# Optimization experiments

Measured on AMD Instinct MI355X. Metric: run time of the kernel, lower is better.

The kernel has to match this reference:

```python
import jax, jax.numpy as jnp
from jax import lax
import numpy as np

EPS = 1e-5
RADIUS = 0.2
NPOINT = 1024
NSAMPLE = 32
B, N = 8, 8192


def furthest_point_sample(xyz, npoint):
    # xyz: (B,N,3) -> idx (B,npoint), start at index 0 (pytorch3d default)
    Bn, Nn, _ = xyz.shape
    def step(carry, _):
        dists, last = carry  # (B,N), (B,)
        lastpt = jnp.take_along_axis(xyz, last[:, None, None], axis=1)  # (B,1,3)
        d = jnp.sum((xyz - lastpt) ** 2, axis=-1)  # (B,N)
        dists = jnp.minimum(dists, d)
        nxt = jnp.argmax(dists, axis=-1).astype(jnp.int32)
        return (dists, nxt), last
    init = (jnp.full((Bn, Nn), jnp.inf, xyz.dtype), jnp.zeros((Bn,), jnp.int32))
    _, idxs = lax.scan(step, init, None, length=npoint)  # (npoint,B)
    return idxs.T  # (B,npoint)


def ball_query(radius, nsample, xyz, new_xyz):
    # first `nsample` points (by original index order) within radius; pad -> 0 (clamp of -1)
    Nn = xyz.shape[1]
    d2 = jnp.sum((new_xyz[:, :, None, :] - xyz[:, None, :, :]) ** 2, axis=-1)  # (B,S,N)
    valid = d2 < radius * radius
    score = jnp.where(valid, jnp.arange(Nn, dtype=jnp.int32), jnp.int32(Nn))  # smaller = earlier valid
    neg_vals, _ = lax.top_k(-score, nsample)  # picks nsample smallest scores
    idx = -neg_vals  # (B,S,nsample)
    idx = jnp.where(idx == Nn, 0, idx)  # pytorch3d pads with -1, then clamp(min=0) -> 0
    return idx


def bn_relu(x, g, be, m, v):
    # eval-mode BatchNorm over channel (last) dim + ReLU
    return jax.nn.relu((x - m) * (g / jnp.sqrt(v + EPS)) + be)


def setup_inputs() -> dict:
    key = jax.random.key(0)
    ks = jax.random.split(key, 4)
    xyz = jax.random.uniform(ks[0], (B, N, 3), dtype=jnp.float32)
    w1 = jax.random.normal(ks[1], (64, 3), dtype=jnp.float32) * 0.1
    w2 = jax.random.normal(ks[2], (64, 64), dtype=jnp.float32) * 0.1
    w3 = jax.random.normal(ks[3], (128, 64), dtype=jnp.float32) * 0.1
    z64, o64 = jnp.zeros((64,), jnp.float32), jnp.ones((64,), jnp.float32)
    z128, o128 = jnp.zeros((128,), jnp.float32), jnp.ones((128,), jnp.float32)
    return {
        "xyz": xyz,
        "w1": w1, "b1": z64, "g1": o64, "be1": z64, "m1": z64, "v1": o64,
        "w2": w2, "b2": z64, "g2": o64, "be2": z64, "m2": z64, "v2": o64,
        "w3": w3, "b3": z128, "g3": o128, "be3": z128, "m3": z128, "v3": o128,
    }


def reference(xyz, w1, b1, g1, be1, m1, v1, w2, b2, g2, be2, m2, v2, w3, b3, g3, be3, m3, v3):
    fps_idx = furthest_point_sample(xyz, NPOINT)  # (B,npoint)
    new_xyz = jnp.take_along_axis(xyz, fps_idx[:, :, None], axis=1)  # (B,npoint,3)
    idx = ball_query(RADIUS, NSAMPLE, xyz, new_xyz)  # (B,npoint,nsample)
    grouped_xyz = jax.vmap(lambda pts, i: pts[i])(xyz, idx)  # (B,npoint,nsample,3)
    # 1x1 conv MLP (channels-last) + eval BN + ReLU
    h = bn_relu(jnp.einsum('bsnc,oc->bsno', grouped_xyz, w1) + b1, g1, be1, m1, v1)
    h = bn_relu(jnp.einsum('bsnc,oc->bsno', h, w2) + b2, g2, be2, m2, v2)
    h = bn_relu(jnp.einsum('bsnc,oc->bsno', h, w3) + b3, g3, be3, m3, v3)
    new_features = jnp.max(h, axis=2)  # (B,npoint,128) max over nsample
    new_features = jnp.transpose(new_features, (0, 2, 1))  # (B,128,npoint) to match torch layout
    return new_xyz, new_features
```

## Files before the change

### kernel.cpp

```cpp
#include <hip/hip_runtime.h>

#define B 8
#define N 8192
#define S 1024
#define NS 32
#define THREADS 256
#define NCONS_BLK 248
#define NCONS_WAVE (NCONS_BLK * 4)
constexpr float BN_EPS = 1e-5f;

typedef float v2f __attribute__((ext_vector_type(2)));

struct KParams {
  const float* xyz;
  const float *w1, *b1, *g1, *be1, *m1, *v1;
  const float *w2, *b2, *g2, *be2, *m2, *v2;
  const float *w3, *b3, *g3, *be3, *m3, *v3;
  float* new_xyz;
  float* out_feat;
  float* ctrs;
  unsigned* prog;
};

__device__ __forceinline__ float wave_max_to_lane63(float x) {
  int v = __float_as_int(x);
#define DPP_MAX(ctrl)                                                     \
  v = __float_as_int(fmaxf(__int_as_float(v),                             \
      __int_as_float(__builtin_amdgcn_update_dpp(v, v, (ctrl), 0xf, 0xf, \
                                                 false))))
  DPP_MAX(0x111);
  DPP_MAX(0x112);
  DPP_MAX(0x114);
  DPP_MAX(0x118);
  DPP_MAX(0x142);
  DPP_MAX(0x143);
#undef DPP_MAX
  return __int_as_float(v);
}

__device__ __forceinline__ void producer(const KParams& P, char* smem, int b,
                                         int t, int lane, int w) {
#pragma clang fp contract(off)
  float4* s_xyz4 = (float4*)smem;
  float* s_ctr = (float*)(smem + 131072);
  unsigned long long(*s_red)[4] =
      (unsigned long long(*)[4])(smem + 131072 + 12288);
  const float* base = P.xyz + (size_t)b * N * 3;
  v2f X[16], Y[16], Z[16], D[16];
  const int p0 = t * 32;
  {
    const float4* src = (const float4*)(base + (size_t)p0 * 3);
    float buf[96];
#pragma unroll
    for (int i = 0; i < 24; ++i) {
      float4 v = src[i];
      buf[4 * i + 0] = v.x; buf[4 * i + 1] = v.y;
      buf[4 * i + 2] = v.z; buf[4 * i + 3] = v.w;
    }
#pragma unroll
    for (int k = 0; k < 32; ++k)
      s_xyz4[p0 + k] =
          make_float4(buf[3 * k], buf[3 * k + 1], buf[3 * k + 2], 0.f);
#pragma unroll
    for (int i = 0; i < 16; ++i) {
      X[i] = (v2f){buf[6 * i + 0], buf[6 * i + 3]};
      Y[i] = (v2f){buf[6 * i + 1], buf[6 * i + 4]};
      Z[i] = (v2f){buf[6 * i + 2], buf[6 * i + 5]};
      D[i] = (v2f){3.4e38f, 3.4e38f};
    }
  }
  float lx = base[0], ly = base[1], lz = base[2];
  if (t == 0) { s_ctr[0] = lx; s_ctr[1] = ly; s_ctr[2] = lz; }
  for (int r = 1; r < S; ++r) {
    v2f lx2 = lx, ly2 = ly, lz2 = lz;
#pragma unroll
    for (int i = 0; i < 16; ++i) {
      v2f dx = X[i] - lx2, dy = Y[i] - ly2, dz = Z[i] - lz2;
      v2f d = (dx * dx + dy * dy) + dz * dz;
      D[i] = __builtin_elementwise_min(D[i], d);
    }
    float n1[16], n2[8], n3[4], n4[2];
#pragma unroll
    for (int i = 0; i < 16; ++i) n1[i] = fmaxf(D[i].x, D[i].y);
#pragma unroll
    for (int i = 0; i < 8; ++i) n2[i] = fmaxf(n1[2 * i], n1[2 * i + 1]);
#pragma unroll
    for (int i = 0; i < 4; ++i) n3[i] = fmaxf(n2[2 * i], n2[2 * i + 1]);
    n4[0] = fmaxf(n3[0], n3[1]);
    n4[1] = fmaxf(n3[2], n3[3]);
    float m = fmaxf(n4[0], n4[1]);
    int c4 = (n4[0] < m) ? 1 : 0;
    float n3s = c4 ? n3[2] : n3[0];
    int c3 = (n3s < m) ? 1 : 0;
    float n2a = c4 ? n2[4] : n2[0];
    float n2b = c4 ? n2[6] : n2[2];
    float n2s = c3 ? n2b : n2a;
    int c2 = (n2s < m) ? 1 : 0;
    float n1a = c4 ? n1[8] : n1[0];
    float n1b = c4 ? n1[10] : n1[2];
    float n1c = c4 ? n1[12] : n1[4];
    float n1d = c4 ? n1[14] : n1[6];
    float n1e = c3 ? n1c : n1a;
    float n1f = c3 ? n1d : n1b;
    float n1s = c2 ? n1f : n1e;
    int c1 = (n1s < m) ? 1 : 0;
    float e0 = c4 ? D[8].x : D[0].x;
    float e1 = c4 ? D[9].x : D[1].x;
    float e2 = c4 ? D[10].x : D[2].x;
    float e3 = c4 ? D[11].x : D[3].x;
    float e4 = c4 ? D[12].x : D[4].x;
    float e5 = c4 ? D[13].x : D[5].x;
    float e6 = c4 ? D[14].x : D[6].x;
    float e7 = c4 ? D[15].x : D[7].x;
    float f0 = c3 ? e4 : e0;
    float f1 = c3 ? e5 : e1;
    float f2 = c3 ? e6 : e2;
    float f3 = c3 ? e7 : e3;
    float g0 = c2 ? f2 : f0;
    float g1 = c2 ? f3 : f1;
    float dxs = c1 ? g1 : g0;
    int c0 = (dxs < m) ? 1 : 0;
    int li = 16 * c4 + 8 * c3 + 4 * c2 + 2 * c1 + c0;
    float wm = wave_max_to_lane63(m);
    float wavemax =
        __int_as_float(__builtin_amdgcn_readlane(__float_as_int(wm), 63));
    unsigned long long bal = __ballot(m == wavemax);
    int firstlane = (int)__builtin_ctzll(bal);
    int widx = __builtin_amdgcn_readlane(p0 + li, firstlane);
    unsigned long long key =
        ((unsigned long long)__float_as_uint(wavemax) << 32) |
        (unsigned)(8191 - widx);
    if (lane == 0) s_red[r & 1][w] = key;
    __syncthreads();
    {
      const unsigned long long* sr = s_red[r & 1];
      unsigned long long k0 = sr[0], k1 = sr[1], k2 = sr[2], k3 = sr[3];
      unsigned long long a = k0 > k1 ? k0 : k1;
      unsigned long long c = k2 > k3 ? k2 : k3;
      unsigned long long kmax = a > c ? a : c;
      const int bi = 8191 - (int)(unsigned)(kmax & 0xffffffffull);
      float4 cc = s_xyz4[bi];
      lx = cc.x; ly = cc.y; lz = cc.z;
    }
    if (t == 0) {
      s_ctr[r * 3 + 0] = lx; s_ctr[r * 3 + 1] = ly; s_ctr[r * 3 + 2] = lz;
    }
    if (w == 0 && (r & 7) == 7) {
      int k8 = r >> 3;
      if (lane == 0 && k8 >= 1)
        __hip_atomic_store(&P.prog[b * 64], (unsigned)(k8 * 8),
                           __ATOMIC_RELEASE, __HIP_MEMORY_SCOPE_AGENT);
      int cbase = (r - 7) * 3;
      if (lane < 24)
        __hip_atomic_store(P.ctrs + (size_t)b * (S * 3) + cbase + lane,
                           s_ctr[cbase + lane], __ATOMIC_RELAXED,
                           __HIP_MEMORY_SCOPE_AGENT);
    }
  }
  __syncthreads();
  if (w == 0 && lane == 0)
    __hip_atomic_store(&P.prog[b * 64], (unsigned)S, __ATOMIC_RELEASE,
                       __HIP_MEMORY_SCOPE_AGENT);
  float* o = P.new_xyz + (size_t)b * S * 3;
  for (int i = t; i < (S * 3) / 4; i += THREADS)
    ((float4*)o)[i] = ((const float4*)s_ctr)[i];
}

__device__ __forceinline__ void consumer(const KParams& P, char* smem, int cid,
                                         int t, int lane, int w) {
#pragma clang fp contract(off)
  constexpr float R2 = (float)(0.2 * 0.2);
  float* h = (float*)smem + w * (NS * 64);
  float* cs = (float*)smem + 4 * NS * 64 + w * (NS * 4);
  const unsigned gw = cid * 4 + w;
  float sv1 = P.g1[lane] / sqrtf(P.v1[lane] + BN_EPS);
  float bb1 = (P.b1[lane] - P.m1[lane]) * sv1 + P.be1[lane];
  float w1x = P.w1[lane * 3 + 0] * sv1, w1y = P.w1[lane * 3 + 1] * sv1,
        w1z = P.w1[lane * 3 + 2] * sv1;
  float sv2 = P.g2[lane] / sqrtf(P.v2[lane] + BN_EPS);
  float bb2 = (P.b2[lane] - P.m2[lane]) * sv2 + P.be2[lane];
  float W2[64];
#pragma unroll
  for (int k = 0; k < 64; k += 4) {
    float4 q = *(const float4*)(P.w2 + lane * 64 + k);
    W2[k + 0] = q.x * sv2; W2[k + 1] = q.y * sv2;
    W2[k + 2] = q.z * sv2; W2[k + 3] = q.w * sv2;
  }
  float sva = P.g3[lane] / sqrtf(P.v3[lane] + BN_EPS);
  float bba = (P.b3[lane] - P.m3[lane]) * sva + P.be3[lane];
  float svb = P.g3[lane + 64] / sqrtf(P.v3[lane + 64] + BN_EPS);
  float bbb = (P.b3[lane + 64] - P.m3[lane + 64]) * svb + P.be3[lane + 64];
  float Wa[64], Wb[64];
#pragma unroll
  for (int k = 0; k < 64; k += 4) {
    float4 qa = *(const float4*)(P.w3 + lane * 64 + k);
    Wa[k + 0] = qa.x * sva; Wa[k + 1] = qa.y * sva;
    Wa[k + 2] = qa.z * sva; Wa[k + 3] = qa.w * sva;
    float4 qb = *(const float4*)(P.w3 + (lane + 64) * 64 + k);
    Wb[k + 0] = qb.x * svb; Wb[k + 1] = qb.y * svb;
    Wb[k + 2] = qb.z * svb; Wb[k + 3] = qb.w * svb;
  }
  for (unsigned c = gw; c < B * S; c += NCONS_WAVE) {
    const int b = c & 7;
    const int s = c >> 3;
    while (__hip_atomic_load(&P.prog[b * 64], __ATOMIC_RELAXED,
                             __HIP_MEMORY_SCOPE_AGENT) <= (unsigned)s)
      __builtin_amdgcn_s_sleep(8);
    (void)__hip_atomic_load(&P.prog[b * 64], __ATOMIC_ACQUIRE,
                            __HIP_MEMORY_SCOPE_AGENT);
    const float* cg = P.ctrs + (size_t)b * (S * 3) + s * 3;
    float cx = __hip_atomic_load(cg + 0, __ATOMIC_RELAXED,
                                 __HIP_MEMORY_SCOPE_AGENT);
    float cy = __hip_atomic_load(cg + 1, __ATOMIC_RELAXED,
                                 __HIP_MEMORY_SCOPE_AGENT);
    float cz = __hip_atomic_load(cg + 2, __ATOMIC_RELAXED,
                                 __HIP_MEMORY_SCOPE_AGENT);
    const float* base = P.xyz + (size_t)b * N * 3;
    int cnt = 0;
    for (int c0 = 0; c0 < N && cnt < NS; c0 += 64) {
      int p = c0 + lane;
      float x = base[p * 3], y = base[p * 3 + 1], z = base[p * 3 + 2];
      float dx = x - cx, dy = y - cy, dz = z - cz;
      float d = (dx * dx + dy * dy) + dz * dz;
      bool v = d < R2;
      unsigned long long mk = __ballot(v);
      int rank = cnt + __popcll(mk & ((1ull << lane) - 1ull));
      if (v && rank < NS) {
        cs[rank * 4 + 0] = x; cs[rank * 4 + 1] = y; cs[rank * 4 + 2] = z;
      }
      cnt += (int)__popcll(mk);
    }
    if (cnt < NS) {
      float x0 = base[0], y0 = base[1], z0 = base[2];
      for (int j = cnt + lane; j < NS; j += 64) {
        cs[j * 4 + 0] = x0; cs[j * 4 + 1] = y0; cs[j * 4 + 2] = z0;
      }
    }
    for (int n = 0; n < NS; ++n) {
      float a = fmaf(w1x, cs[n * 4 + 0],
                     fmaf(w1y, cs[n * 4 + 1], fmaf(w1z, cs[n * 4 + 2], bb1)));
      h[n * 64 + lane] = fmaxf(a, 0.f);
    }
    for (int n = 0; n < NS; ++n) {
      float acc = bb2;
#pragma unroll
      for (int k = 0; k < 64; k += 4) {
        float4 q = *(const float4*)(h + n * 64 + k);
        acc = fmaf(W2[k + 0], q.x, acc);
        acc = fmaf(W2[k + 1], q.y, acc);
        acc = fmaf(W2[k + 2], q.z, acc);
        acc = fmaf(W2[k + 3], q.w, acc);
      }
      h[n * 64 + lane] = fmaxf(acc, 0.f);
    }
    float mxa = 0.f, mxb = 0.f;
    for (int n = 0; n < NS; ++n) {
      float acca = bba, accb = bbb;
#pragma unroll
      for (int k = 0; k < 64; k += 4) {
        float4 q = *(const float4*)(h + n * 64 + k);
        acca = fmaf(Wa[k + 0], q.x, acca);
        acca = fmaf(Wa[k + 1], q.y, acca);
        acca = fmaf(Wa[k + 2], q.z, acca);
        acca = fmaf(Wa[k + 3], q.w, acca);
        accb = fmaf(Wb[k + 0], q.x, accb);
        accb = fmaf(Wb[k + 1], q.y, accb);
        accb = fmaf(Wb[k + 2], q.z, accb);
        accb = fmaf(Wb[k + 3], q.w, accb);
      }
      mxa = fmaxf(mxa, acca);
      mxb = fmaxf(mxb, accb);
    }
    P.out_feat[((size_t)b * 128 + lane) * S + s] = mxa;
    P.out_feat[((size_t)b * 128 + 64 + lane) * S + s] = mxb;
  }
}

__global__ void __attribute__((amdgpu_flat_work_group_size(THREADS, THREADS),
                               amdgpu_waves_per_eu(1, 1)))
k_fused(KParams P) {
  extern __shared__ char smem[];
  const int t = threadIdx.x;
  const int lane = t & 63;
  const int w = t >> 6;
  if (blockIdx.x < B)
    producer(P, smem, blockIdx.x, t, lane, w);
  else
    consumer(P, smem, blockIdx.x - B, t, lane, w);
}

extern "C" void kernel_launch(void* const* d_in, const int* in_sizes, int n_in,
                              void* d_out, int out_size, void* d_ws,
                              size_t ws_size, hipStream_t stream) {
  KParams P;
  P.xyz = (const float*)d_in[0];
  P.w1 = (const float*)d_in[1];  P.b1 = (const float*)d_in[2];
  P.g1 = (const float*)d_in[3];  P.be1 = (const float*)d_in[4];
  P.m1 = (const float*)d_in[5];  P.v1 = (const float*)d_in[6];
  P.w2 = (const float*)d_in[7];  P.b2 = (const float*)d_in[8];
  P.g2 = (const float*)d_in[9];  P.be2 = (const float*)d_in[10];
  P.m2 = (const float*)d_in[11]; P.v2 = (const float*)d_in[12];
  P.w3 = (const float*)d_in[13]; P.b3 = (const float*)d_in[14];
  P.g3 = (const float*)d_in[15]; P.be3 = (const float*)d_in[16];
  P.m3 = (const float*)d_in[17]; P.v3 = (const float*)d_in[18];
  float* out = (float*)d_out;
  P.new_xyz = out;
  P.out_feat = out + (size_t)B * S * 3;
  P.prog = (unsigned*)d_ws;
  P.ctrs = (float*)((char*)d_ws + 2048);

  hipMemsetAsync(d_ws, 0, 2048, stream);

  void* args[] = {&P};
  dim3 grid(B + NCONS_BLK), blk(THREADS);
  size_t shmem = 131072 + 12288 + 256;
  hipError_t e = hipLaunchCooperativeKernel((const void*)k_fused, grid, blk,
                                            args, (unsigned)shmem, stream);
  if (e != hipSuccess) {
    k_fused<<<grid, blk, shmem, stream>>>(P);
  }
}
```

Measured before the change: 950.4 us.

## Replace per-iteration block barrier in FPS with tagged LDS spin-wait reduction

Each FPS iteration's workgroup __syncthreads is replaced by a flag-free exchange: every wave writes a key tagged with the iteration number to LDS, then spins with acquire loads until the other three waves' keys carry the same tag, and each wave computes the argmax itself. The point index is packed into 13 bits alongside the tag, and the key still orders by distance first. This removes a full barrier from the 1023-step serial critical path at the cost of spin traffic on LDS. The cooperative launch is also dropped for a plain launch, which no longer guarantees co-residency for the producer/consumer progress waits.

```diff
diff --git a/kernel.cpp b/kernel.cpp
--- a/kernel.cpp
+++ b/kernel.cpp
@@ -43,8 +43,8 @@
 #pragma clang fp contract(off)
   float4* s_xyz4 = (float4*)smem;
   float* s_ctr = (float*)(smem + 131072);
-  unsigned long long(*s_red)[4] =
-      (unsigned long long(*)[4])(smem + 131072 + 12288);
+  unsigned long long* s_red =
+      (unsigned long long*)(smem + 131072 + 12288);
   const float* base = P.xyz + (size_t)b * N * 3;
   v2f X[16], Y[16], Z[16], D[16];
   const int p0 = t * 32;
@@ -69,8 +69,10 @@
       D[i] = (v2f){3.4e38f, 3.4e38f};
     }
   }
+  __syncthreads();
   float lx = base[0], ly = base[1], lz = base[2];
   if (t == 0) { s_ctr[0] = lx; s_ctr[1] = ly; s_ctr[2] = lz; }
+  const int j1 = (w + 1) & 3, j2 = (w + 2) & 3, j3 = (w + 3) & 3;
   for (int r = 1; r < S; ++r) {
     v2f lx2 = lx, ly2 = ly, lz2 = lz;
 #pragma unroll
@@ -127,21 +129,31 @@
     unsigned long long bal = __ballot(m == wavemax);
     int firstlane = (int)__builtin_ctzll(bal);
     int widx = __builtin_amdgcn_readlane(p0 + li, firstlane);
+    const unsigned tag = (unsigned)r & 0x1fffu;
     unsigned long long key =
         ((unsigned long long)__float_as_uint(wavemax) << 32) |
-        (unsigned)(8191 - widx);
-    if (lane == 0) s_red[r & 1][w] = key;
-    __syncthreads();
-    {
-      const unsigned long long* sr = s_red[r & 1];
-      unsigned long long k0 = sr[0], k1 = sr[1], k2 = sr[2], k3 = sr[3];
-      unsigned long long a = k0 > k1 ? k0 : k1;
-      unsigned long long c = k2 > k3 ? k2 : k3;
-      unsigned long long kmax = a > c ? a : c;
-      const int bi = 8191 - (int)(unsigned)(kmax & 0xffffffffull);
-      float4 cc = s_xyz4[bi];
-      lx = cc.x; ly = cc.y; lz = cc.z;
-    }
+        ((unsigned)(8191 - widx) << 13) | tag;
+    unsigned long long* sr = s_red + (r & 1) * 4;
+    if (lane == 0)
+      __hip_atomic_store(&sr[w], key, __ATOMIC_RELEASE,
+                         __HIP_MEMORY_SCOPE_WORKGROUP);
+    unsigned long long ka, kb, kc;
+    do {
+      ka = __hip_atomic_load(&sr[j1], __ATOMIC_ACQUIRE,
+                             __HIP_MEMORY_SCOPE_WORKGROUP);
+      kb = __hip_atomic_load(&sr[j2], __ATOMIC_ACQUIRE,
+                             __HIP_MEMORY_SCOPE_WORKGROUP);
+      kc = __hip_atomic_load(&sr[j3], __ATOMIC_ACQUIRE,
+                             __HIP_MEMORY_SCOPE_WORKGROUP);
+    } while ((((unsigned)ka ^ tag) & 0x1fffu) |
+             (((unsigned)kb ^ tag) & 0x1fffu) |
+             (((unsigned)kc ^ tag) & 0x1fffu));
+    unsigned long long kmax = key > ka ? key : ka;
+    unsigned long long kcd = kb > kc ? kb : kc;
+    kmax = kmax > kcd ? kmax : kcd;
+    const int bi = 8191 - (int)(((unsigned)kmax >> 13) & 0x1fffu);
+    float4 cc = s_xyz4[bi];
+    lx = cc.x; ly = cc.y; lz = cc.z;
     if (t == 0) {
       s_ctr[r * 3 + 0] = lx; s_ctr[r * 3 + 1] = ly; s_ctr[r * 3 + 2] = lz;
     }
@@ -311,12 +323,7 @@
 
   hipMemsetAsync(d_ws, 0, 2048, stream);
 
-  void* args[] = {&P};
   dim3 grid(B + NCONS_BLK), blk(THREADS);
   size_t shmem = 131072 + 12288 + 256;
-  hipError_t e = hipLaunchCooperativeKernel((const void*)k_fused, grid, blk,
-                                            args, (unsigned)shmem, stream);
-  if (e != hipSuccess) {
-    k_fused<<<grid, blk, shmem, stream>>>(P);
-  }
-}
+  k_fused<<<grid, blk, shmem, stream>>>(P);
+}
```

Measured after the change: 997.8 us. 5.0% more time.
